# Performance work log

Measured on AMD Instinct MI355X. Metric: run time of the kernel, lower is better.

Reference implementation:

```python
import jax, jax.numpy as jnp
import numpy as np


def build_masks(H, W):
    """The 16 shifted-window masks (0 inside window, -inf outside), matching torch code."""
    m = np.full((16, H, W), -np.inf, dtype=np.float32)
    h2, w2 = int(H / 2), int(W / 2)
    for i in range(4):
        hs, ws = int(H * (i / 8)), int(W * (i / 8))
        k = 4 * i
        # mask1
        m[k + 0, hs:h2 + hs, ws:w2 + ws] = 0.0
        # mask2
        m[k + 1, hs:h2 + hs, w2 + ws:W + ws] = 0.0
        m[k + 1, hs:h2 + hs, 0:ws] = 0.0
        # mask3
        m[k + 2, h2 + hs:H + hs, ws:w2 + ws] = 0.0
        m[k + 2, 0:hs, ws:w2 + ws] = 0.0
        # mask4
        m[k + 3, h2 + hs:H + hs, w2 + ws:W + ws] = 0.0
        m[k + 3, 0:hs, 0:ws] = 0.0
        m[k + 3, h2 + hs:H + hs, 0:ws] = 0.0
        m[k + 3, 0:hs, w2 + ws:W + ws] = 0.0
    return jnp.asarray(m)


def setup_inputs() -> dict:
    key = jax.random.key(0)
    k1, k2 = jax.random.split(key)
    x = jax.random.normal(k1, (8, 512, 128, 128), dtype=jnp.float32)
    w = jax.random.normal(k2, (512,), dtype=jnp.float32) * 0.02  # 1x1 conv weight, out_ch=1
    return {"input": x, "w_conv": w}


def reference(input, w_conv):
    B, C, H, W = input.shape
    # 1x1 bias-free conv 512 -> 1 is a channel dot product -> [B, H, W]
    x = jnp.einsum('bchw,c->bhw', input, w_conv)
    masks = build_masks(H, W)  # [16, H, W] constants
    # Broadcast-add all 16 masks, softmax over the flattened H*W (exp(-inf)=0)
    logits = (x[:, None, :, :] + masks[None]).reshape(B, 16, H * W)
    p = jax.nn.softmax(logits, axis=-1).reshape(B, 16, H, W)
    swin_att = p.sum(axis=1)[:, None, :, :]  # [B, 1, H, W]
    return swin_att * input + input
```

## Files before the change

### kernel.cpp

```cpp
#include <hip/hip_runtime.h>
#include <hip/hip_bf16.h>
#include <math.h>

#define B   8
#define C   512
#define H   128
#define W   128
#define HW  16384
#define HWQ 4096
#define BHW 131072
#define NCHUNK 8
#define CPC    64

typedef float  nfloat4 __attribute__((ext_vector_type(4)));

__global__ __launch_bounds__(256)
void conv_partial_kernel(const float* __restrict__ in,
                         const float* __restrict__ wv,
                         float* __restrict__ partial) {
    int t = blockIdx.x * 256 + threadIdx.x;
    int chunk = t >> 15;
    int quad  = t & 32767;
    int b = quad >> 12;
    int q = quad & (HWQ - 1);

    const float4* inp = (const float4*)in
        + (size_t)b * (C * HWQ)
        + (size_t)chunk * CPC * HWQ
        + q;
    const float* wc = wv + chunk * CPC;

    float4 acc = make_float4(0.f, 0.f, 0.f, 0.f);
#pragma unroll 8
    for (int c = 0; c < CPC; ++c) {
        float4 v = inp[(size_t)c * HWQ];
        float wcc = wc[c];
        acc.x += v.x * wcc;
        acc.y += v.y * wcc;
        acc.z += v.z * wcc;
        acc.w += v.w * wcc;
    }
    ((float4*)partial)[(size_t)chunk * 32768 + quad] = acc;
}

__global__ __launch_bounds__(256)
void reduce_partial_kernel(const float4* __restrict__ partial,
                           float4* __restrict__ xproj) {
    int t = blockIdx.x * 256 + threadIdx.x;
    float4 s = make_float4(0.f, 0.f, 0.f, 0.f);
#pragma unroll
    for (int ch = 0; ch < NCHUNK; ++ch) {
        float4 p = partial[(size_t)ch * (BHW / 4) + t];
        s.x += p.x;
        s.y += p.y;
        s.z += p.z;
        s.w += p.w;
    }
    xproj[t] = s;
}

__global__ __launch_bounds__(256)
void stats_kernel(const float* __restrict__ xproj,
                  float* __restrict__ coef) {
    int bk = blockIdx.x;
    int b = bk >> 4, k = bk & 15;
    int i = k >> 2, j = k & 3;
    int h0 = (16 * i + ((j >> 1) ? 64 : 0)) & (H - 1);
    int w0 = (16 * i + ((j & 1) ? 64 : 0)) & (W - 1);
    const float* x = xproj + b * HW;

    int tid = threadIdx.x;
    float v[16];
    float m = -1e30f;
#pragma unroll
    for (int it = 0; it < 16; ++it) {
        int p = tid + 256 * it;
        int r = p >> 6, c = p & 63;
        int h = (h0 + r) & (H - 1);
        int w = (w0 + c) & (W - 1);
        v[it] = x[h * W + w];
        m = fmaxf(m, v[it]);
    }
    for (int off = 32; off > 0; off >>= 1)
        m = fmaxf(m, __shfl_down(m, off, 64));
    __shared__ float sm[4];
    __shared__ float ss[4];
    int lane = tid & 63, wv = tid >> 6;
    if (lane == 0) sm[wv] = m;
    __syncthreads();
    m = fmaxf(fmaxf(sm[0], sm[1]), fmaxf(sm[2], sm[3]));

    float s = 0.f;
#pragma unroll
    for (int it = 0; it < 16; ++it)
        s += expf(v[it] - m);
    for (int off = 32; off > 0; off >>= 1)
        s += __shfl_down(s, off, 64);
    if (lane == 0) ss[wv] = s;
    __syncthreads();
    if (tid == 0) {
        float Z = ss[0] + ss[1] + ss[2] + ss[3];
        coef[bk] = expf(-m) / Z;
    }
}

__global__ __launch_bounds__(256)
void scale_kernel(const float* __restrict__ xproj,
                  const float* __restrict__ coef,
                  float* __restrict__ scale) {
    int t = blockIdx.x * 256 + threadIdx.x;
    int b = t >> 14;
    int hw = t & (HW - 1);
    int h = hw >> 7, w = hw & (W - 1);
    const float* cf = coef + b * 16;
    float acc = 0.f;
#pragma unroll
    for (int i = 0; i < 4; ++i) {
        int hr = (h - 16 * i) & (H - 1);
        int wr = (w - 16 * i) & (W - 1);
        int idx = 4 * i + ((hr < 64) ? 0 : 2) + ((wr < 64) ? 0 : 1);
        acc += cf[idx];
    }
    scale[t] = 1.0f + expf(xproj[t]) * acc;
}

__global__ __launch_bounds__(256)
void apply_kernel(const float4* __restrict__ in,
                  const float4* __restrict__ scale,
                  float4* __restrict__ out) {
    size_t base = (size_t)(gridDim.x - 1 - blockIdx.x) * 256;
    size_t t = base + threadIdx.x;
    float4 v = in[t];
    int b = (int)(t >> 21);
    int q = (int)(t & (HWQ - 1));
    float4 s = scale[((size_t)b << 12) + q];
    nfloat4 r;
    r.x = v.x * s.x;
    r.y = v.y * s.y;
    r.z = v.z * s.z;
    r.w = v.w * s.w;
    __builtin_nontemporal_store(r, (nfloat4*)&out[t]);
}

extern "C" void kernel_launch(void* const* d_in, const int* in_sizes, int n_in,
                              void* d_out, int out_size, void* d_ws, size_t ws_size,
                              hipStream_t stream) {
    const float* input  = (const float*)d_in[0];
    const float* w_conv = (const float*)d_in[1];
    float* out = (float*)d_out;

    float* ws      = (float*)d_ws;
    float* partial = ws;
    float* xproj   = ws + (size_t)NCHUNK * BHW;
    float* coef    = xproj + BHW;
    float* scale   = coef + 128;

    conv_partial_kernel<<<1024, 256, 0, stream>>>(input, w_conv, partial);
    reduce_partial_kernel<<<BHW / 1024, 256, 0, stream>>>(
        (const float4*)partial, (float4*)xproj);
    stats_kernel<<<B * 16, 256, 0, stream>>>(xproj, coef);
    scale_kernel<<<BHW / 256, 256, 0, stream>>>(xproj, coef, scale);
    apply_kernel<<<(B * C * HW / 4) / 256, 256, 0, stream>>>(
        (const float4*)input, (const float4*)scale, (float4*)out);
}
```

Baseline: 472.9 us.

## Fuse all stages into one cooperative kernel with grid syncs

```diff
diff --git a/kernel.cpp b/kernel.cpp
--- a/kernel.cpp
+++ b/kernel.cpp
@@ -1,6 +1,8 @@
 #include <hip/hip_runtime.h>
-#include <hip/hip_bf16.h>
+#include <hip/hip_cooperative_groups.h>
 #include <math.h>
+
+namespace cg = cooperative_groups;
 
 #define B   8
 #define C   512
@@ -12,134 +14,147 @@
 #define NCHUNK 8
 #define CPC    64
 
-typedef float  nfloat4 __attribute__((ext_vector_type(4)));
+typedef float nfloat4 __attribute__((ext_vector_type(4)));
 
-__global__ __launch_bounds__(256)
-void conv_partial_kernel(const float* __restrict__ in,
-                         const float* __restrict__ wv,
-                         float* __restrict__ partial) {
-    int t = blockIdx.x * 256 + threadIdx.x;
-    int chunk = t >> 15;
-    int quad  = t & 32767;
-    int b = quad >> 12;
-    int q = quad & (HWQ - 1);
-
-    const float4* inp = (const float4*)in
-        + (size_t)b * (C * HWQ)
-        + (size_t)chunk * CPC * HWQ
-        + q;
-    const float* wc = wv + chunk * CPC;
-
-    float4 acc = make_float4(0.f, 0.f, 0.f, 0.f);
-#pragma unroll 8
-    for (int c = 0; c < CPC; ++c) {
-        float4 v = inp[(size_t)c * HWQ];
-        float wcc = wc[c];
-        acc.x += v.x * wcc;
-        acc.y += v.y * wcc;
-        acc.z += v.z * wcc;
-        acc.w += v.w * wcc;
-    }
-    ((float4*)partial)[(size_t)chunk * 32768 + quad] = acc;
-}
-
-__global__ __launch_bounds__(256)
-void reduce_partial_kernel(const float4* __restrict__ partial,
-                           float4* __restrict__ xproj) {
-    int t = blockIdx.x * 256 + threadIdx.x;
-    float4 s = make_float4(0.f, 0.f, 0.f, 0.f);
-#pragma unroll
-    for (int ch = 0; ch < NCHUNK; ++ch) {
-        float4 p = partial[(size_t)ch * (BHW / 4) + t];
-        s.x += p.x;
-        s.y += p.y;
-        s.z += p.z;
-        s.w += p.w;
-    }
-    xproj[t] = s;
-}
-
-__global__ __launch_bounds__(256)
-void stats_kernel(const float* __restrict__ xproj,
-                  float* __restrict__ coef) {
-    int bk = blockIdx.x;
-    int b = bk >> 4, k = bk & 15;
-    int i = k >> 2, j = k & 3;
-    int h0 = (16 * i + ((j >> 1) ? 64 : 0)) & (H - 1);
-    int w0 = (16 * i + ((j & 1) ? 64 : 0)) & (W - 1);
-    const float* x = xproj + b * HW;
-
-    int tid = threadIdx.x;
-    float v[16];
-    float m = -1e30f;
-#pragma unroll
-    for (int it = 0; it < 16; ++it) {
-        int p = tid + 256 * it;
-        int r = p >> 6, c = p & 63;
-        int h = (h0 + r) & (H - 1);
-        int w = (w0 + c) & (W - 1);
-        v[it] = x[h * W + w];
-        m = fmaxf(m, v[it]);
-    }
-    for (int off = 32; off > 0; off >>= 1)
-        m = fmaxf(m, __shfl_down(m, off, 64));
+__global__ __launch_bounds__(256, 4)
+void fused_kernel(const float* __restrict__ in,
+                  const float* __restrict__ wv,
+                  float* __restrict__ partial,
+                  float* __restrict__ xproj,
+                  float* __restrict__ coef,
+                  float* __restrict__ out) {
+    cg::grid_group grid = cg::this_grid();
     __shared__ float sm[4];
     __shared__ float ss[4];
-    int lane = tid & 63, wv = tid >> 6;
-    if (lane == 0) sm[wv] = m;
-    __syncthreads();
-    m = fmaxf(fmaxf(sm[0], sm[1]), fmaxf(sm[2], sm[3]));
 
-    float s = 0.f;
+    const int tid = threadIdx.x;
+    const int t   = blockIdx.x * 256 + tid;
+
+    {
+        int chunk = t >> 15;
+        int quad  = t & 32767;
+        int b = quad >> 12;
+        int q = quad & (HWQ - 1);
+
+        const float4* inp = (const float4*)in
+            + (size_t)b * (C * HWQ)
+            + (size_t)chunk * CPC * HWQ
+            + q;
+        const float* wc = wv + chunk * CPC;
+
+        float4 acc = make_float4(0.f, 0.f, 0.f, 0.f);
+#pragma unroll 8
+        for (int c = 0; c < CPC; ++c) {
+            float4 v = inp[(size_t)c * HWQ];
+            float wcc = wc[c];
+            acc.x += v.x * wcc;
+            acc.y += v.y * wcc;
+            acc.z += v.z * wcc;
+            acc.w += v.w * wcc;
+        }
+        ((float4*)partial)[(size_t)chunk * 32768 + quad] = acc;
+    }
+    grid.sync();
+
+    if (blockIdx.x < 128) {
+        int u = blockIdx.x * 256 + tid;
+        float4 s = make_float4(0.f, 0.f, 0.f, 0.f);
 #pragma unroll
-    for (int it = 0; it < 16; ++it)
-        s += expf(v[it] - m);
-    for (int off = 32; off > 0; off >>= 1)
-        s += __shfl_down(s, off, 64);
-    if (lane == 0) ss[wv] = s;
-    __syncthreads();
-    if (tid == 0) {
-        float Z = ss[0] + ss[1] + ss[2] + ss[3];
-        coef[bk] = expf(-m) / Z;
+        for (int ch = 0; ch < NCHUNK; ++ch) {
+            float4 p = ((const float4*)partial)[(size_t)ch * 32768 + u];
+            s.x += p.x;
+            s.y += p.y;
+            s.z += p.z;
+            s.w += p.w;
+        }
+        ((float4*)xproj)[u] = s;
     }
-}
+    grid.sync();
 
-__global__ __launch_bounds__(256)
-void scale_kernel(const float* __restrict__ xproj,
-                  const float* __restrict__ coef,
-                  float* __restrict__ scale) {
-    int t = blockIdx.x * 256 + threadIdx.x;
-    int b = t >> 14;
-    int hw = t & (HW - 1);
-    int h = hw >> 7, w = hw & (W - 1);
-    const float* cf = coef + b * 16;
-    float acc = 0.f;
+    if (blockIdx.x < 128) {
+        int bk = blockIdx.x;
+        int b = bk >> 4, k = bk & 15;
+        int i = k >> 2, j = k & 3;
+        int h0 = (16 * i + ((j >> 1) ? 64 : 0)) & (H - 1);
+        int w0 = (16 * i + ((j & 1) ? 64 : 0)) & (W - 1);
+        const float* x = xproj + b * HW;
+
+        float v[16];
+        float m = -1e30f;
 #pragma unroll
-    for (int i = 0; i < 4; ++i) {
-        int hr = (h - 16 * i) & (H - 1);
-        int wr = (w - 16 * i) & (W - 1);
-        int idx = 4 * i + ((hr < 64) ? 0 : 2) + ((wr < 64) ? 0 : 1);
-        acc += cf[idx];
+        for (int it = 0; it < 16; ++it) {
+            int p = tid + 256 * it;
+            int r = p >> 6, c = p & 63;
+            int h = (h0 + r) & (H - 1);
+            int w = (w0 + c) & (W - 1);
+            v[it] = x[h * W + w];
+            m = fmaxf(m, v[it]);
+        }
+        for (int off = 32; off > 0; off >>= 1)
+            m = fmaxf(m, __shfl_down(m, off, 64));
+        int lane = tid & 63, wvi = tid >> 6;
+        if (lane == 0) sm[wvi] = m;
+        __syncthreads();
+        m = fmaxf(fmaxf(sm[0], sm[1]), fmaxf(sm[2], sm[3]));
+
+        float s = 0.f;
+#pragma unroll
+        for (int it = 0; it < 16; ++it)
+            s += expf(v[it] - m);
+        for (int off = 32; off > 0; off >>= 1)
+            s += __shfl_down(s, off, 64);
+        if (lane == 0) ss[wvi] = s;
+        __syncthreads();
+        if (tid == 0) {
+            float Z = ss[0] + ss[1] + ss[2] + ss[3];
+            coef[bk] = expf(-m) / Z;
+        }
     }
-    scale[t] = 1.0f + expf(xproj[t]) * acc;
-}
+    grid.sync();
 
-__global__ __launch_bounds__(256)
-void apply_kernel(const float4* __restrict__ in,
-                  const float4* __restrict__ scale,
-                  float4* __restrict__ out) {
-    size_t base = (size_t)(gridDim.x - 1 - blockIdx.x) * 256;
-    size_t t = base + threadIdx.x;
-    float4 v = in[t];
-    int b = (int)(t >> 21);
-    int q = (int)(t & (HWQ - 1));
-    float4 s = scale[((size_t)b << 12) + q];
-    nfloat4 r;
-    r.x = v.x * s.x;
-    r.y = v.y * s.y;
-    r.z = v.z * s.z;
-    r.w = v.w * s.w;
-    __builtin_nontemporal_store(r, (nfloat4*)&out[t]);
+    {
+        int q    = t & (HWQ - 1);
+        int cofs = t >> 12;
+        int h  = q >> 5;
+        int w0 = (q & 31) * 4;
+
+        for (int b = B - 1; b >= 0; --b) {
+            const float* cf = coef + b * 16;
+            float4 xp = ((const float4*)xproj)[(b << 12) + q];
+
+            float a0 = 0.f, a1 = 0.f, a2 = 0.f, a3 = 0.f;
+#pragma unroll
+            for (int i = 0; i < 4; ++i) {
+                int hr = (h - 16 * i) & (H - 1);
+                int hterm = 4 * i + ((hr < 64) ? 0 : 2);
+                int wr0 = (w0 + 0 - 16 * i) & (W - 1);
+                int wr1 = (w0 + 1 - 16 * i) & (W - 1);
+                int wr2 = (w0 + 2 - 16 * i) & (W - 1);
+                int wr3 = (w0 + 3 - 16 * i) & (W - 1);
+                a0 += cf[hterm + ((wr0 < 64) ? 0 : 1)];
+                a1 += cf[hterm + ((wr1 < 64) ? 0 : 1)];
+                a2 += cf[hterm + ((wr2 < 64) ? 0 : 1)];
+                a3 += cf[hterm + ((wr3 < 64) ? 0 : 1)];
+            }
+            float4 s4;
+            s4.x = 1.0f + expf(xp.x) * a0;
+            s4.y = 1.0f + expf(xp.y) * a1;
+            s4.z = 1.0f + expf(xp.z) * a2;
+            s4.w = 1.0f + expf(xp.w) * a3;
+
+            for (int band = 7; band >= 0; --band) {
+                int c = band * 64 + cofs;
+                size_t g = ((size_t)(b * C + c) << 12) + q;
+                float4 v = ((const float4*)in)[g];
+                nfloat4 r;
+                r.x = v.x * s4.x;
+                r.y = v.y * s4.y;
+                r.z = v.z * s4.z;
+                r.w = v.w * s4.w;
+                __builtin_nontemporal_store(r, (nfloat4*)((float4*)out + g));
+            }
+        }
+    }
 }
 
 extern "C" void kernel_launch(void* const* d_in, const int* in_sizes, int n_in,
@@ -153,13 +168,11 @@
     float* partial = ws;
     float* xproj   = ws + (size_t)NCHUNK * BHW;
     float* coef    = xproj + BHW;
-    float* scale   = coef + 128;
 
-    conv_partial_kernel<<<1024, 256, 0, stream>>>(input, w_conv, partial);
-    reduce_partial_kernel<<<BHW / 1024, 256, 0, stream>>>(
-        (const float4*)partial, (float4*)xproj);
-    stats_kernel<<<B * 16, 256, 0, stream>>>(xproj, coef);
-    scale_kernel<<<BHW / 256, 256, 0, stream>>>(xproj, coef, scale);
-    apply_kernel<<<(B * C * HW / 4) / 256, 256, 0, stream>>>(
-        (const float4*)input, (const float4*)scale, (float4*)out);
+    void* args[] = {
+        (void*)&input, (void*)&w_conv, (void*)&partial,
+        (void*)&xproj, (void*)&coef, (void*)&out
+    };
+    hipLaunchCooperativeKernel((const void*)fused_kernel,
+                               dim3(1024), dim3(256), args, 0, stream);
 }
```

Result: slower. 812.1 us (+71.7%).
